# Kernel tuning notes

Hardware: AMD Instinct MI355X
Metric: run time of the kernel (lower is better)

The kernel has to match this reference:

```python
import jax, jax.numpy as jnp
import numpy as np

# ---- dims ----
V, VR, E, H, NF = 100000, 5000, 300, 256, 150
H2 = 2 * H  # 512


def _lstm_dir(x, Wih, Whh, b, h0, c0):
    # x: (T, B, E); returns hs (T, B, H), final (h, c)
    def step(carry, xt):
        h, c = carry
        z = xt @ Wih.T + h @ Whh.T + b
        i, f, g, o = jnp.split(z, 4, axis=-1)  # torch gate order i,f,g,o
        c = jax.nn.sigmoid(f) * c + jax.nn.sigmoid(i) * jnp.tanh(g)
        h = jax.nn.sigmoid(o) * jnp.tanh(c)
        return (h, c), h
    (hT, cT), hs = jax.lax.scan(step, (h0, c0), x)
    return hs, hT, cT


def bilstm(x, Wih_f, Whh_f, b_f, Wih_b, Whh_b, b_b, state=None):
    # x: (T, B, E) -> out (T, B, 2H), state tuple
    B = x.shape[1]
    if state is None:
        z = jnp.zeros((B, H), x.dtype)
        state = (z, z, z, z)
    h0f, c0f, h0b, c0b = state
    hs_f, hTf, cTf = _lstm_dir(x, Wih_f, Whh_f, b_f, h0f, c0f)
    hs_b, hTb, cTb = _lstm_dir(x[::-1], Wih_b, Whh_b, b_b, h0b, c0b)
    out = jnp.concatenate([hs_f, hs_b[::-1]], axis=-1)
    return out, (hTf, cTf, hTb, cTb)


def abwim_atten(question_out, word_rel, rela_rel, word_emb, rela_emb,
                Wih_f, Whh_f, b_f, Wih_b, Whh_b, b_b, W):
    # question_out: (B, 2H, Sq); word_rel (B,Sw), rela_rel (B,Sr) int
    rela = rela_emb[rela_rel.T]   # (Sr, B, E)
    word = word_emb[word_rel.T]   # (Sw, B, E)
    word_out, state = bilstm(word, Wih_f, Whh_f, b_f, Wih_b, Whh_b, b_b)
    rela_out, _ = bilstm(rela, Wih_f, Whh_f, b_f, Wih_b, Whh_b, b_b, state)
    relation = jnp.concatenate([rela_out, word_out], axis=0).transpose(1, 0, 2)  # (B, R, 2H)
    energy = jnp.einsum('brh,hk,bks->brs', relation, W, question_out)  # (B, R, Sq)
    B, R, Sq = energy.shape
    scale = 1.0 / np.sqrt(R).astype(np.float32)
    alpha = jax.nn.softmax(energy.reshape(B, R * Sq) * scale, axis=-1).reshape(B, R, Sq)
    # sum_r alpha[b,r,s] * relation[b,r,h] -> (B, 2H, Sq)
    return jnp.einsum('brs,brh->bhs', alpha, relation)


def setup_inputs():
    key = jax.random.key(0)
    ks = jax.random.split(key, 24)
    B, Sq, Sw, Sr = 64, 40, 12, 4
    s_emb, s_lstm, s_w = 0.05, 0.05, 0.04
    inp = {
        'question': jax.random.randint(ks[0], (B, Sq), 0, V),
        'word_relation': jax.random.randint(ks[1], (B, Sw), 0, V),
        'rela_relation': jax.random.randint(ks[2], (B, Sr), 0, VR),
        'word_previous': jax.random.randint(ks[3], (B, Sw), 0, V),
        'rela_previous': jax.random.randint(ks[4], (B, Sr), 0, VR),
        'word_emb': jax.random.normal(ks[5], (V, E), jnp.float32) * s_emb,
        'rela_emb': jax.random.normal(ks[6], (VR, E), jnp.float32) * s_emb,
        'Wih_f': jax.random.normal(ks[7], (4 * H, E), jnp.float32) * s_lstm,
        'Whh_f': jax.random.normal(ks[8], (4 * H, H), jnp.float32) * s_lstm,
        'b_f': jnp.zeros((4 * H,), jnp.float32),
        'Wih_b': jax.random.normal(ks[9], (4 * H, E), jnp.float32) * s_lstm,
        'Whh_b': jax.random.normal(ks[10], (4 * H, H), jnp.float32) * s_lstm,
        'b_b': jnp.zeros((4 * H,), jnp.float32),
        'W': jax.random.normal(ks[11], (H2, H2), jnp.float32) * s_w,
        'cnn1_w': jax.random.normal(ks[12], (NF, 2 * H2, 1), jnp.float32) * s_w,
        'cnn1_b': jnp.zeros((NF,), jnp.float32),
        'cnn2_w': jax.random.normal(ks[13], (NF, 2 * H2, 3), jnp.float32) * s_w,
        'cnn2_b': jnp.zeros((NF,), jnp.float32),
        'cnn3_w': jax.random.normal(ks[14], (NF, 2 * H2, 5), jnp.float32) * s_w,
        'cnn3_b': jnp.zeros((NF,), jnp.float32),
        'lin_w': jax.random.normal(ks[15], (1, NF), jnp.float32) * s_w,
        'lin2_w': jax.random.normal(ks[16], (H2, H2), jnp.float32) * s_w,
        'lin2_b': jnp.zeros((H2,), jnp.float32),
    }
    return inp


def _conv1d(x, w, b):
    # x: (B, C, L), w: (O, C, K)
    y = jax.lax.conv_general_dilated(x, w, (1,), 'VALID',
                                     dimension_numbers=('NCH', 'OIH', 'NCH'))
    return y + b[None, :, None]


def reference(question, word_relation, rela_relation, word_previous, rela_previous,
              word_emb, rela_emb, Wih_f, Whh_f, b_f, Wih_b, Whh_b, b_b, W,
              cnn1_w, cnn1_b, cnn2_w, cnn2_b, cnn3_w, cnn3_b, lin_w, lin2_w, lin2_b):
    lstm_p = (Wih_f, Whh_f, b_f, Wih_b, Whh_b, b_b)
    # question encoder (dropout is identity at eval)
    q = word_emb[question.T]                      # (Sq, B, E)
    q_out, _ = bilstm(q, *lstm_p)                 # (Sq, B, 2H)
    question_out = q_out.transpose(1, 2, 0)       # (B, 2H, Sq)
    # reduce one previous hop
    atten_prev = abwim_atten(question_out, word_previous, rela_previous,
                             word_emb, rela_emb, *lstm_p, W)
    qo = question_out - atten_prev
    qo = qo.transpose(0, 2, 1) @ lin2_w.T + lin2_b   # (B, Sq, 2H)
    question_out = qo.transpose(0, 2, 1)             # (B, 2H, Sq)
    # current relation attention
    atten_relation = abwim_atten(question_out, word_relation, rela_relation,
                                 word_emb, rela_emb, *lstm_p, W)
    M = jnp.concatenate([question_out, atten_relation], axis=1)  # (B, 4H, Sq)
    h1 = jnp.max(jax.nn.relu(_conv1d(M, cnn1_w, cnn1_b)), axis=2)  # (B, NF)
    h2 = jnp.max(jax.nn.relu(_conv1d(M, cnn2_w, cnn2_b)), axis=2)
    h3 = jnp.max(jax.nn.relu(_conv1d(M, cnn3_w, cnn3_b)), axis=2)
    h = jnp.maximum(jnp.maximum(h1, h2), h3)
    score = (h @ lin_w.T).squeeze(-1)  # (B,)
    return score
```

## Files before the change

### kernel.cpp

```cpp
#include <hip/hip_runtime.h>
#include <math.h>

#define NEG_INF (-3.402823466e+38f)

typedef __attribute__((ext_vector_type(8))) short short8;
typedef __attribute__((ext_vector_type(8))) unsigned short ushort8;
typedef __attribute__((ext_vector_type(4))) float f32x4;

constexpr int NTOK = 4608;
constexpr int BH = 64 * 256;

constexpr size_t OFF_WQ    = 0;
constexpr size_t OFF_B2    = OFF_WQ    + 524288;
constexpr size_t OFF_XB3T  = OFF_B2    + 2048;
constexpr size_t OFF_WB3T  = OFF_XB3T  + 983040;
constexpr size_t OFF_L2B3T = OFF_WB3T  + 393216;
constexpr size_t OFF_C1B3T = OFF_L2B3T + 393216;
constexpr size_t OFF_C2B3T = OFF_C1B3T + 294912;
constexpr size_t OFF_C3B3T = OFF_C2B3T + 884736;
constexpr size_t OFF_XHI   = OFF_C3B3T + 1474560;
constexpr size_t OFF_XLO   = OFF_XHI   + 737280;
constexpr size_t OFF_XP    = OFF_XLO   + 737280;
constexpr size_t OFF_HSQ   = OFF_XP    + 9437184;
constexpr size_t OFF_HSWP  = OFF_HSQ   + 1310720;
constexpr size_t OFF_HSRP  = OFF_HSWP  + 393216;
constexpr size_t OFF_HSWR  = OFF_HSRP  + 131072;
constexpr size_t OFF_HSRR  = OFF_HSWR  + 393216;
constexpr size_t OFF_CS    = OFF_HSRR  + 131072;
constexpr size_t OFF_RELP  = OFF_CS    + 163840;
constexpr size_t OFF_RELC  = OFF_RELP  + 524288;
constexpr size_t OFF_RELW  = OFF_RELC  + 524288;
constexpr size_t OFF_EN    = OFF_RELW  + 524288;

__device__ inline unsigned short f2bf(float f) {
  unsigned int u = __float_as_uint(f);
  u += 0x7FFFu + ((u >> 16) & 1u);
  return (unsigned short)(u >> 16);
}
__device__ inline float bf2f(unsigned short h) {
  return __uint_as_float(((unsigned int)h) << 16);
}
__device__ inline short8 mk8(unsigned long long a, unsigned long long b) {
  union { unsigned long long q[2]; short8 s; } u;
  u.q[0] = a; u.q[1] = b; return u.s;
}
#define ALD(p) __hip_atomic_load((p), __ATOMIC_RELAXED, __HIP_MEMORY_SCOPE_AGENT)
#define AST(p, v) __hip_atomic_store((p), (v), __ATOMIC_RELAXED, __HIP_MEMORY_SCOPE_AGENT)

__global__ __launch_bounds__(256) void k_prep(
    const float* __restrict__ Whh_f, const float* __restrict__ Whh_b,
    const float* __restrict__ b_f,   const float* __restrict__ b_b,
    const float* __restrict__ Wih_f, const float* __restrict__ Wih_b,
    const float* __restrict__ Wat,   const float* __restrict__ l2w,
    const float* __restrict__ c1w, const float* __restrict__ c2w, const float* __restrict__ c3w,
    unsigned short* __restrict__ WHB, float* __restrict__ B2,
    unsigned short* __restrict__ XB3T, unsigned short* __restrict__ WB3T,
    unsigned short* __restrict__ L2B3T,
    unsigned short* __restrict__ C1B3T, unsigned short* __restrict__ C2B3T,
    unsigned short* __restrict__ C3B3T, int* __restrict__ flags) {
  int idx = blockIdx.x * 256 + threadIdx.x;
  if (idx < 3072)
    AST(flags + idx * 16, 0);
  else if (idx < 3200)
    AST(flags + 49152 + (idx - 3072) * 16, 0);
  if (idx < 1048576) {
    int e = idx & 511;
    int k = e & 255, isLo = e >> 8;
    int row = (idx >> 9) & 63;
    int tile = (idx >> 15) & 15;
    int d = idx >> 19;
    int g = row >> 4, uu = row & 15;
    int u = tile * 16 + uu;
    const float* Wh = d ? Whh_b : Whh_f;
    float w = Wh[(size_t)(g * 256 + u) * 256 + k];
    unsigned short hi = f2bf(w);
    WHB[idx] = isLo ? f2bf(w - bf2f(hi)) : hi;
    return;
  }
  idx -= 1048576;
  if (idx < 2048) { B2[idx] = (idx < 1024) ? b_f[idx] : b_b[idx-1024]; return; }
  idx -= 2048;
  unsigned short* dst; int n, k, K;
  float w;
  if (idx < 655360) {
    n = idx / 320; k = idx % 320; K = 320; dst = XB3T;
    w = (k < 300) ? ((n < 1024) ? Wih_f[(size_t)n*300 + k] : Wih_b[(size_t)(n-1024)*300 + k]) : 0.f;
  } else if ((idx -= 655360) < 262144) {
    n = idx >> 9; k = idx & 511; K = 512; dst = WB3T;
    w = Wat[(size_t)k*512 + n];
  } else if ((idx -= 262144) < 262144) {
    n = idx >> 9; k = idx & 511; K = 512; dst = L2B3T;
    w = l2w[(size_t)n*512 + k];
  } else if ((idx -= 262144) < 196608) {
    n = idx >> 10; k = idx & 1023; K = 1024; dst = C1B3T;
    w = (n < 150) ? c1w[(size_t)n*1024 + k] : 0.f;
  } else if ((idx -= 196608) < 589824) {
    n = idx / 3072; k = idx % 3072; K = 3072; dst = C2B3T;
    int kw = k >> 10, c = k & 1023;
    w = (n < 150) ? c2w[((size_t)n*1024 + c)*3 + kw] : 0.f;
  } else if ((idx -= 589824) < 983040) {
    n = idx / 5120; k = idx % 5120; K = 5120; dst = C3B3T;
    int kw = k >> 10, c = k & 1023;
    w = (n < 150) ? c3w[((size_t)n*1024 + c)*5 + kw] : 0.f;
  } else return;
  unsigned short hi = f2bf(w);
  unsigned short lo = f2bf(w - bf2f(hi));
  size_t base = (size_t)n * (3*K);
  dst[base + k] = hi;
  dst[base + K + k] = lo;
  dst[base + 2*K + k] = hi;
}

__global__ __launch_bounds__(320) void k_gather(
    const int* __restrict__ q,  const int* __restrict__ wr, const int* __restrict__ rr,
    const int* __restrict__ wp, const int* __restrict__ rp,
    const float* __restrict__ we, const float* __restrict__ re,
    unsigned short* __restrict__ Xhi, unsigned short* __restrict__ Xlo) {
  int m = blockIdx.x, k = threadIdx.x;
  const float* emb; int row;
  if (m < 2560)      { int t=m>>6,    b=m&63; row = q [b*40+t]; emb = we; }
  else if (m < 3328) { int mm=m-2560; int t=mm>>6,b=mm&63; row = wp[b*12+t]; emb = we; }
  else if (m < 3584) { int mm=m-3328; int t=mm>>6,b=mm&63; row = rp[b*4 +t]; emb = re; }
  else if (m < 4352) { int mm=m-3584; int t=mm>>6,b=mm&63; row = wr[b*12+t]; emb = we; }
  else               { int mm=m-4352; int t=mm>>6,b=mm&63; row = rr[b*4 +t]; emb = re; }
  float v = (k < 300) ? emb[(size_t)row*300 + k] : 0.f;
  unsigned short hi = f2bf(v);
  Xhi[(size_t)m*320 + k] = hi;
  Xlo[(size_t)m*320 + k] = f2bf(v - bf2f(hi));
}

template<bool BIAS>
__global__ __launch_bounds__(256) void k_mgemm(
    const unsigned short* __restrict__ Ahi, const unsigned short* __restrict__ Alo, int lda,
    const unsigned short* __restrict__ Bt, const float* __restrict__ bias,
    float* __restrict__ C, int N, int K) {
  __shared__ unsigned short As[64 * 40];
  __shared__ unsigned short Bs[64 * 40];
  int tid = threadIdx.x;
  int wave = tid >> 6, lane = tid & 63;
  int quad = lane >> 4, l16 = lane & 15;
  int m0 = blockIdx.x << 6, n0 = blockIdx.y << 6;
  int K3 = 3 * K;
  int sr = tid >> 2;
  int sc = (tid & 3) << 3;
  f32x4 acc[4] = {};
  for (int k0 = 0; k0 < K3; k0 += 32) {
    int c = (k0 >= K) + (k0 >= 2*K);
    const unsigned short* Asrc = (c == 2) ? Alo : Ahi;
    int kk = k0 - c * K;
    ushort8 av = *(const ushort8*)(Asrc + (size_t)(m0 + sr) * lda + kk + sc);
    ushort8 bv = *(const ushort8*)(Bt + (size_t)(n0 + sr) * K3 + k0 + sc);
    *(ushort8*)&As[sr * 40 + sc] = av;
    *(ushort8*)&Bs[sr * 40 + sc] = bv;
    __syncthreads();
    short8 a  = *(const short8*)&As[(wave*16 + l16) * 40 + quad*8];
    short8 b0 = *(const short8*)&Bs[( 0 + l16) * 40 + quad*8];
    short8 b1 = *(const short8*)&Bs[(16 + l16) * 40 + quad*8];
    short8 b2 = *(const short8*)&Bs[(32 + l16) * 40 + quad*8];
    short8 b3 = *(const short8*)&Bs[(48 + l16) * 40 + quad*8];
    acc[0] = __builtin_amdgcn_mfma_f32_16x16x32_bf16(a, b0, acc[0], 0, 0, 0);
    acc[1] = __builtin_amdgcn_mfma_f32_16x16x32_bf16(a, b1, acc[1], 0, 0, 0);
    acc[2] = __builtin_amdgcn_mfma_f32_16x16x32_bf16(a, b2, acc[2], 0, 0, 0);
    acc[3] = __builtin_amdgcn_mfma_f32_16x16x32_bf16(a, b3, acc[3], 0, 0, 0);
    __syncthreads();
  }
  int row0 = m0 + wave * 16 + quad * 4;
#pragma unroll
  for (int t = 0; t < 4; t++) {
    int col = n0 + t * 16 + l16;
    float bb = BIAS ? bias[col] : 0.f;
#pragma unroll
    for (int r = 0; r < 4; r++)
      C[(size_t)(row0 + r) * N + col] = acc[t][r] + bb;
  }
}

__global__ __launch_bounds__(256) void k_cgemm(
    const unsigned short* __restrict__ Ahi, const unsigned short* __restrict__ Alo,
    const unsigned short* __restrict__ B1, const unsigned short* __restrict__ B2c,
    const unsigned short* __restrict__ B3,
    float* __restrict__ Y1, float* __restrict__ Y2, float* __restrict__ Y3) {
  __shared__ unsigned short As[64 * 40];
  __shared__ unsigned short Bs[64 * 40];
  int z = blockIdx.z;
  const unsigned short* Bt; float* Y; int K, sidx, chunk;
  if (z < 4)       { Bt = B1;  Y = Y1; K = 1024; sidx = z;      chunk = 768;  }
  else if (z < 12) { Bt = B2c; Y = Y2; K = 3072; sidx = z - 4;  chunk = 1152; }
  else             { Bt = B3;  Y = Y3; K = 5120; sidx = z - 12; chunk = 1920; }
  int K3 = 3 * K;
  int ks = sidx * chunk, ke = ks + chunk;
  int tid = threadIdx.x;
  int wave = tid >> 6, lane = tid & 63;
  int quad = lane >> 4, l16 = lane & 15;
  int m0 = blockIdx.x << 6, n0 = blockIdx.y << 6;
  int sr = tid >> 2;
  int sc = (tid & 3) << 3;
  f32x4 acc[4] = {};
  for (int k0 = ks; k0 < ke; k0 += 32) {
    int c = (k0 >= K) + (k0 >= 2*K);
    const unsigned short* Asrc = (c == 2) ? Alo : Ahi;
    int kk = k0 - c * K;
    ushort8 av = *(const ushort8*)(Asrc + (size_t)(m0 + sr) * 1024 + kk + sc);
    ushort8 bv = *(const ushort8*)(Bt + (size_t)(n0 + sr) * K3 + k0 + sc);
    *(ushort8*)&As[sr * 40 + sc] = av;
    *(ushort8*)&Bs[sr * 40 + sc] = bv;
    __syncthreads();
    short8 a  = *(const short8*)&As[(wave*16 + l16) * 40 + quad*8];
    short8 b0 = *(const short8*)&Bs[( 0 + l16) * 40 + quad*8];
    short8 b1 = *(const short8*)&Bs[(16 + l16) * 40 + quad*8];
    short8 b2 = *(const short8*)&Bs[(32 + l16) * 40 + quad*8];
    short8 b3 = *(const short8*)&Bs[(48 + l16) * 40 + quad*8];
    acc[0] = __builtin_amdgcn_mfma_f32_16x16x32_bf16(a, b0, acc[0], 0, 0, 0);
    acc[1] = __builtin_amdgcn_mfma_f32_16x16x32_bf16(a, b1, acc[1], 0, 0, 0);
    acc[2] = __builtin_amdgcn_mfma_f32_16x16x32_bf16(a, b2, acc[2], 0, 0, 0);
    acc[3] = __builtin_amdgcn_mfma_f32_16x16x32_bf16(a, b3, acc[3], 0, 0, 0);
    __syncthreads();
  }
  int row0 = m0 + wave * 16 + quad * 4;
#pragma unroll
  for (int t = 0; t < 4; t++) {
    int col = n0 + t * 16 + l16;
#pragma unroll
    for (int r = 0; r < 4; r++)
      atomicAdd(&Y[(size_t)(row0 + r) * 192 + col], acc[t][r]);
  }
}

__global__ __launch_bounds__(256) void k_zero(float* __restrict__ p, int n4) {
  int idx = blockIdx.x * 256 + threadIdx.x;
  if (idx < n4) *(float4*)(p + (size_t)idx * 4) = make_float4(0.f, 0.f, 0.f, 0.f);
}

__global__ __launch_bounds__(256, 1) void k_steps(
    const unsigned short* __restrict__ WHB, const float* __restrict__ XP,
    float* __restrict__ hsQ, float* __restrict__ hsWp, float* __restrict__ hsRp,
    float* __restrict__ hsWr, float* __restrict__ hsRr,
    unsigned short* HxA, unsigned short* HxB,
    int* flags, int* det) {
  int bid = blockIdx.x;
  int chain = bid & 7;
  if (chain >= 6) return;
  int tile = bid >> 3;
  int dir = chain & 1, fam = chain >> 1;
  int tid = threadIdx.x;
  int wave = tid >> 6, lane = tid & 63;
  int quad = lane >> 4, l16 = lane & 15;
  int u0 = tile << 4;

  unsigned myxcd;
  asm volatile("s_getreg_b32 %0, hwreg(HW_REG_XCC_ID)" : "=s"(myxcd));
  if (tid == 0) AST(det + bid * 16, (int)myxcd + 1);

  const unsigned short* wsrc = WHB + (((size_t)dir * 16 + tile) << 15);
  short8 Bh[4][8], Bl[4][8];
#pragma unroll
  for (int nf = 0; nf < 4; nf++)
#pragma unroll
    for (int j = 0; j < 8; j++) {
      const unsigned short* wr = wsrc + (nf * 16 + l16) * 512 + j * 32 + quad * 8;
      Bh[nf][j] = *(const short8*)(wr);
      Bl[nf][j] = *(const short8*)(wr + 256);
    }

  __shared__ int s_fast;
  int idv = 0;
  if (tid < 16) {
    const int* dp = det + (tid * 8 + chain) * 16;
    int v;
    while ((v = ALD(dp)) == 0) __builtin_amdgcn_s_sleep(1);
    idv = v;
  }
  if (wave == 0) {
    int ref = __shfl(idv, 0, 64);
    unsigned long long bad = __ballot((lane < 16) && (idv != ref));
    if (lane == 0) s_fast = (bad == 0ULL);
  }
  __syncthreads();
  int fast = s_fast;

  int nsteps = (fam == 0) ? 40 : 16;
  int slot0 = (chain < 2) ? chain * 40 : 80 + (chain - 2) * 16;
  float creg[4] = {0.f, 0.f, 0.f, 0.f};
  int roff = (quad * 64 + wave * 16 + l16) * 8;
  int wj = tile >> 1;
  int wq = ((tile & 1) << 1) + (l16 >> 3);
  int wbase = ((wj * 4 + wq) * 64) * 4 + ((l16 & 7) >> 1);

  for (int cs = 0; cs < nsteps; cs++) {
    int t, T, seg; float* hsb;
    if (fam == 0)     { t = cs;      T = 40; seg = 0;                         hsb = hsQ + (size_t)dir * 40 * BH; }
    else if (cs < 12) { t = cs;      T = 12; seg = (fam == 1) ? 2560 : 3584;  hsb = ((fam == 1) ? hsWp : hsWr) + (size_t)dir * 12 * BH; }
    else              { t = cs - 12; T = 4;  seg = (fam == 1) ? 3328 : 4352;  hsb = ((fam == 1) ? hsRp : hsRr) + (size_t)dir * 4 * BH; }
    int t_in = dir ? (T - 1 - t) : t;
    int u = u0 + l16;
    const float* xb = XP + (size_t)(seg + t_in * 64) * 2048 + dir * 1024 + u;
    float xi[4], xf[4], xg[4], xo[4];
#pragma unroll
    for (int r = 0; r < 4; r++) {
      const float* xr = xb + (size_t)(wave * 16 + quad * 4 + r) * 2048;
      xi[r] = xr[0]; xf[r] = xr[256]; xg[r] = xr[512]; xo[r] = xr[768];
    }

    f32x4 acc[4] = {};
    if (cs > 0) {
      int rs = slot0 + cs - 1;
      const unsigned short* Hb = (rs < 96) ? (HxA + (size_t)rs * 32768)
                                           : (HxB + (size_t)(rs - 96) * 32768);
      if (tid < 16) {
        const int* fp = flags + ((rs * 16 + tid) << 4);
        while (ALD(fp) == 0) __builtin_amdgcn_s_sleep(1);
      }
      __syncthreads();
      short8 ah[8], al[8];
      if (fast) {
#pragma unroll
        for (int j = 0; j < 8; j++) {
          ah[j] = *(const short8*)(Hb + j * 2048 + roff);
          al[j] = *(const short8*)(Hb + 16384 + j * 2048 + roff);
        }
      } else {
        const unsigned long long* ph = (const unsigned long long*)Hb;
        const unsigned long long* pl = ph + 4096;
        int r4 = roff >> 2;
        unsigned long long rv[32];
#pragma unroll
        for (int j = 0; j < 8; j++) { rv[2*j] = ALD(ph + j*512 + r4); rv[2*j+1] = ALD(ph + j*512 + r4 + 1); }
#pragma unroll
        for (int j = 0; j < 8; j++) { rv[16+2*j] = ALD(pl + j*512 + r4); rv[16+2*j+1] = ALD(pl + j*512 + r4 + 1); }
#pragma unroll
        for (int j = 0; j < 8; j++) { ah[j] = mk8(rv[2*j], rv[2*j+1]); al[j] = mk8(rv[16+2*j], rv[16+2*j+1]); }
      }
#pragma unroll
      for (int j = 0; j < 8; j++) {
        acc[0] = __builtin_amdgcn_mfma_f32_16x16x32_bf16(ah[j], Bh[0][j], acc[0], 0, 0, 0);
        acc[1] = __builtin_amdgcn_mfma_f32_16x16x32_bf16(ah[j], Bh[1][j], acc[1], 0, 0, 0);
        acc[2] = __builtin_amdgcn_mfma_f32_16x16x32_bf16(ah[j], Bh[2][j], acc[2], 0, 0, 0);
        acc[3] = __builtin_amdgcn_mfma_f32_16x16x32_bf16(ah[j], Bh[3][j], acc[3], 0, 0, 0);
      }
#pragma unroll
      for (int j = 0; j < 8; j++) {
        acc[0] = __builtin_amdgcn_mfma_f32_16x16x32_bf16(ah[j], Bl[0][j], acc[0], 0, 0, 0);
        acc[1] = __builtin_amdgcn_mfma_f32_16x16x32_bf16(ah[j], Bl[1][j], acc[1], 0, 0, 0);
        acc[2] = __builtin_amdgcn_mfma_f32_16x16x32_bf16(ah[j], Bl[2][j], acc[2], 0, 0, 0);
        acc[3] = __builtin_amdgcn_mfma_f32_16x16x32_bf16(ah[j], Bl[3][j], acc[3], 0, 0, 0);
      }
#pragma unroll
      for (int j = 0; j < 8; j++) {
        acc[0] = __builtin_amdgcn_mfma_f32_16x16x32_bf16(al[j], Bh[0][j], acc[0], 0, 0, 0);
        acc[1] = __builtin_amdgcn_mfma_f32_16x16x32_bf16(al[j], Bh[1][j], acc[1], 0, 0, 0);
        acc[2] = __builtin_amdgcn_mfma_f32_16x16x32_bf16(al[j], Bh[2][j], acc[2], 0, 0, 0);
        acc[3] = __builtin_amdgcn_mfma_f32_16x16x32_bf16(al[j], Bh[3][j], acc[3], 0, 0, 0);
      }
    }
    float hnv[4];
#pragma unroll
    for (int r = 0; r < 4; r++) {
      float zi = acc[0][r] + xi[r];
      float zf = acc[1][r] + xf[r];
      float zg = acc[2][r] + xg[r];
      float zo = acc[3][r] + xo[r];
      float gi = 1.f / (1.f + expf(-zi));
      float gf = 1.f / (1.f + expf(-zf));
      float go = 1.f / (1.f + expf(-zo));
      float gg = tanhf(zg);
      float cn = gf * creg[r] + gi * gg;
      hnv[r] = go * tanhf(cn);
      creg[r] = cn;
    }
    int wslot = slot0 + cs;
    if (cs + 1 < nsteps) {
      unsigned short* Ho = (wslot < 96) ? (HxA + (size_t)wslot * 32768)
                                        : (HxB + (size_t)(wslot - 96) * 32768);
      unsigned int* ohw = (unsigned int*)Ho + wbase;
      unsigned int* olw = (unsigned int*)(Ho + 16384) + wbase;
#pragma unroll
      for (int r = 0; r < 4; r++) {
        int b = wave * 16 + quad * 4 + r;
        unsigned short h16 = f2bf(hnv[r]);
        unsigned short l16v = f2bf(hnv[r] - bf2f(h16));
        unsigned int pk = (unsigned int)h16 | ((unsigned int)l16v << 16);
        unsigned int pw = (unsigned int)__shfl_xor((int)pk, 1, 64);
        if ((lane & 1) == 0) {
          unsigned int hw = (pk & 0xFFFFu) | (pw << 16);
          unsigned int lw = (pk >> 16) | (pw & 0xFFFF0000u);
          if (fast) { ohw[b * 4] = hw; olw[b * 4] = lw; }
          else      { AST(ohw + b * 4, hw); AST(olw + b * 4, lw); }
        }
      }
      __syncthreads();
      if (tid == 0)
        AST(flags + ((wslot * 16 + tile) << 4), 1);
    }
    float* hout = hsb + (size_t)t * BH + u;
#pragma unroll
    for (int r = 0; r < 4; r++) {
      int b = wave * 16 + quad * 4 + r;
      hout[(size_t)b * 256] = hnv[r];
    }
  }
}

__global__ __launch_bounds__(256) void k_qo1(const float* __restrict__ hsQ, float* __restrict__ QT) {
  int idx = blockIdx.x * 256 + threadIdx.x;
  if (idx >= 64*40*512) return;
  int h = idx & 511; int t2 = idx >> 9; int s = t2 % 40; int b = t2 / 40;
  float v;
  if (h < 256) v = hsQ[(size_t)s * BH + b*256 + h];
  else         v = hsQ[(size_t)40 * BH + (size_t)(39 - s) * BH + b*256 + (h - 256)];
  QT[idx] = v;
}

__global__ __launch_bounds__(256) void k_rel(
    const float* __restrict__ hsWp, const float* __restrict__ hsRp,
    const float* __restrict__ hsWr, const float* __restrict__ hsRr,
    float* __restrict__ RELP, float* __restrict__ RELC,
    unsigned short* __restrict__ RPhi, unsigned short* __restrict__ RPlo,
    unsigned short* __restrict__ RChi, unsigned short* __restrict__ RClo) {
  int idx0 = blockIdx.x * 256 + threadIdx.x;
  if (idx0 >= 2*64*16*512) return;
  int call = idx0 >= 64*16*512;
  int idx = idx0 - call * 64*16*512;
  int h = idx & 511; int t2 = idx >> 9; int r = t2 & 15; int b = t2 >> 4;
  const float* hsW = call ? hsWr : hsWp;
  const float* hsR = call ? hsRr : hsRp;
  float v;
  if (r < 4) {
    if (h < 256) v = hsR[(size_t)r * BH + b*256 + h];
    else         v = hsR[(size_t)4 * BH + (size_t)(3 - r) * BH + b*256 + (h - 256)];
  } else {
    int t = r - 4;
    if (h < 256) v = hsW[(size_t)t * BH + b*256 + h];
    else         v = hsW[(size_t)12 * BH + (size_t)(11 - t) * BH + b*256 + (h - 256)];
  }
  unsigned short hi = f2bf(v);
  unsigned short lo = f2bf(v - bf2f(hi));
  if (call) { RELC[idx] = v; RChi[idx] = hi; RClo[idx] = lo; }
  else      { RELP[idx] = v; RPhi[idx] = hi; RPlo[idx] = lo; }
}

__global__ __launch_bounds__(256) void k_energy(
    const float* __restrict__ relW, const float* __restrict__ QT, float* __restrict__ EN) {
  int idx = blockIdx.x * 256 + threadIdx.x;
  if (idx >= 64*16*40) return;
  int s = idx % 40; int t = idx / 40; int r = t & 15; int b = t >> 4;
  const float* rw = relW + (size_t)(b*16 + r) * 512;
  const float* qv = QT   + (size_t)(b*40 + s) * 512;
  float acc = 0.f;
#pragma unroll 4
  for (int k = 0; k < 512; k += 4) {
    float4 a = *(const float4*)(rw + k);
    float4 c = *(const float4*)(qv + k);
    acc += a.x*c.x + a.y*c.y + a.z*c.z + a.w*c.w;
  }
  EN[idx] = acc;
}

__global__ __launch_bounds__(256) void k_softmax(float* __restrict__ EN) {
  int b = blockIdx.x; int tid = threadIdx.x;
  float* e = EN + b * 640;
  float v0 = e[tid] * 0.25f, v1 = e[tid + 256] * 0.25f;
  float v2 = (tid < 128) ? e[tid + 512] * 0.25f : NEG_INF;
  __shared__ float sh[256];
  sh[tid] = fmaxf(v0, fmaxf(v1, v2));
  __syncthreads();
  for (int st = 128; st > 0; st >>= 1) { if (tid < st) sh[tid] = fmaxf(sh[tid], sh[tid+st]); __syncthreads(); }
  float m = sh[0];
  __syncthreads();
  float e0 = expf(v0 - m), e1 = expf(v1 - m);
  float e2 = (tid < 128) ? expf(v2 - m) : 0.f;
  sh[tid] = e0 + e1 + e2;
  __syncthreads();
  for (int st = 128; st > 0; st >>= 1) { if (tid < st) sh[tid] += sh[tid+st]; __syncthreads(); }
  float inv = 1.f / sh[0];
  e[tid] = e0 * inv; e[tid + 256] = e1 * inv;
  if (tid < 128) e[tid + 512] = e2 * inv;
}

__global__ __launch_bounds__(256) void k_atten(
    const float* __restrict__ AL, const float* __restrict__ REL, float* __restrict__ ATT) {
  int idx = blockIdx.x * 256 + threadIdx.x;
  if (idx >= 64*40*512) return;
  int h = idx & 511; int t2 = idx >> 9; int s = t2 % 40; int b = t2 / 40;
  const float* al = AL + b * 640 + s;
  const float* rl = REL + (size_t)b * 16 * 512 + h;
  float acc = 0.f;
#pragma unroll
  for (int r = 0; r < 16; r++) acc += al[r*40] * rl[r*512];
  ATT[idx] = acc;
}

__global__ __launch_bounds__(256) void k_sub(
    const float* __restrict__ QT, const float* __restrict__ ATT,
    unsigned short* __restrict__ Dhi, unsigned short* __restrict__ Dlo) {
  int idx = blockIdx.x * 256 + threadIdx.x;
  if (idx >= 64*40*512) return;
  float v = QT[idx] - ATT[idx];
  unsigned short hi = f2bf(v);
  Dhi[idx] = hi; Dlo[idx] = f2bf(v - bf2f(hi));
}

__global__ __launch_bounds__(256) void k_m2(
    const float* __restrict__ QO2, const float* __restrict__ ATT,
    unsigned short* __restrict__ M2hi, unsigned short* __restrict__ M2lo) {
  int idx = blockIdx.x * 256 + threadIdx.x;
  if (idx >= 2626048) return;
  float v = 0.f;
  if (idx < 2621440) {
    int c = idx & 1023; int m = idx >> 10;
    v = (c < 512) ? QO2[(size_t)m*512 + c] : ATT[(size_t)m*512 + (c - 512)];
  }
  unsigned short hi = f2bf(v);
  M2hi[idx] = hi; M2lo[idx] = f2bf(v - bf2f(hi));
}

__global__ __launch_bounds__(256) void k_pool(
    const float* __restrict__ Y1, const float* __restrict__ Y2, const float* __restrict__ Y3,
    const float* __restrict__ b1, const float* __restrict__ b2, const float* __restrict__ b3,
    const float* __restrict__ lw, float* __restrict__ out) {
  int b = blockIdx.x, o = threadIdx.x;
  float hv = 0.f;
  if (o < 150) {
    const float* y1 = Y1 + (size_t)b*40*192 + o;
    const float* y2 = Y2 + (size_t)b*40*192 + o;
    const float* y3 = Y3 + (size_t)b*40*192 + o;
    float m1 = NEG_INF, m2 = NEG_INF, m3 = NEG_INF;
#pragma unroll 4
    for (int l = 0; l < 40; l++) m1 = fmaxf(m1, y1[l*192]);
#pragma unroll 2
    for (int l = 0; l < 38; l++) m2 = fmaxf(m2, y2[l*192]);
#pragma unroll 2
    for (int l = 0; l < 36; l++) m3 = fmaxf(m3, y3[l*192]);
    float h = fmaxf(fmaxf(m1 + b1[o], m2 + b2[o]), m3 + b3[o]);
    hv = fmaxf(h, 0.f) * lw[o];
  }
  __shared__ float sh[256];
  sh[threadIdx.x] = hv;
  __syncthreads();
  for (int st = 128; st > 0; st >>= 1) { if (threadIdx.x < st) sh[threadIdx.x] += sh[threadIdx.x+st]; __syncthreads(); }
  if (threadIdx.x == 0) out[b] = sh[0];
}

extern "C" void kernel_launch(void* const* d_in, const int* in_sizes, int n_in,
                              void* d_out, int out_size, void* d_ws, size_t ws_size,
                              hipStream_t stream) {
  const int*   q    = (const int*)d_in[0];
  const int*   wrel = (const int*)d_in[1];
  const int*   rrel = (const int*)d_in[2];
  const int*   wprv = (const int*)d_in[3];
  const int*   rprv = (const int*)d_in[4];
  const float* we   = (const float*)d_in[5];
  const float* re   = (const float*)d_in[6];
  const float* Wih_f= (const float*)d_in[7];
  const float* Whh_f= (const float*)d_in[8];
  const float* b_f  = (const float*)d_in[9];
  const float* Wih_b= (const float*)d_in[10];
  const float* Whh_b= (const float*)d_in[11];
  const float* b_b  = (const float*)d_in[12];
  const float* W    = (const float*)d_in[13];
  const float* c1w  = (const float*)d_in[14];
  const float* c1b  = (const float*)d_in[15];
  const float* c2w  = (const float*)d_in[16];
  const float* c2b  = (const float*)d_in[17];
  const float* c3w  = (const float*)d_in[18];
  const float* c3b  = (const float*)d_in[19];
  const float* lw   = (const float*)d_in[20];
  const float* l2w  = (const float*)d_in[21];
  const float* l2b  = (const float*)d_in[22];
  float* out = (float*)d_out;
  float* ws  = (float*)d_ws;

  unsigned short* WHB = (unsigned short*)(ws + OFF_WQ);
  float* B2   = ws + OFF_B2;
  unsigned short* XB3T  = (unsigned short*)(ws + OFF_XB3T);
  unsigned short* WB3T  = (unsigned short*)(ws + OFF_WB3T);
  unsigned short* L2B3T = (unsigned short*)(ws + OFF_L2B3T);
  unsigned short* C1B3T = (unsigned short*)(ws + OFF_C1B3T);
  unsigned short* C2B3T = (unsigned short*)(ws + OFF_C2B3T);
  unsigned short* C3B3T = (unsigned short*)(ws + OFF_C3B3T);
  unsigned short* Xhi   = (unsigned short*)(ws + OFF_XHI);
  unsigned short* Xlo   = (unsigned short*)(ws + OFF_XLO);
  float* XP   = ws + OFF_XP;
  float* HSQ  = ws + OFF_HSQ;
  float* HSWP = ws + OFF_HSWP;
  float* HSRP = ws + OFF_HSRP;
  float* HSWR = ws + OFF_HSWR;
  float* HSRR = ws + OFF_HSRR;
  int*   flags = (int*)(ws + OFF_CS);
  int*   det   = flags + 49152;
  float* RELP = ws + OFF_RELP;
  float* RELC = ws + OFF_RELC;
  float* RELW = ws + OFF_RELW;
  float* EN   = ws + OFF_EN;
  unsigned short* HxA = (unsigned short*)(ws + OFF_RELP);
  unsigned short* HxB = (unsigned short*)(ws + OFF_XB3T);
  float* QO1  = XP;
  float* ATT  = XP + 1310720;
  float* QO2  = XP + 2621440;
  unsigned short* Dhi  = (unsigned short*)(XP + 3932160);
  unsigned short* Dlo  = (unsigned short*)(XP + 4587520);
  unsigned short* RPhi = (unsigned short*)(XP + 5242880);
  unsigned short* RPlo = (unsigned short*)(XP + 5505024);
  unsigned short* RChi = (unsigned short*)(XP + 5767168);
  unsigned short* RClo = (unsigned short*)(XP + 6029312);
  unsigned short* M2hi = (unsigned short*)(XP + 5242880);
  unsigned short* M2lo = (unsigned short*)(XP + 6555904);
  float* Y1   = XP + 7868928;
  float* Y2   = XP + 8360448;
  float* Y3   = XP + 8851968;

  k_prep<<<15624, 256, 0, stream>>>(Whh_f, Whh_b, b_f, b_b, Wih_f, Wih_b, W, l2w,
                                    c1w, c2w, c3w,
                                    WHB, B2, XB3T, WB3T, L2B3T, C1B3T, C2B3T, C3B3T, flags);
  k_gather<<<NTOK, 320, 0, stream>>>(q, wrel, rrel, wprv, rprv, we, re, Xhi, Xlo);
  { dim3 g(72, 32); k_mgemm<true><<<g, 256, 0, stream>>>(Xhi, Xlo, 320, XB3T, B2, XP, 2048, 320); }

  k_steps<<<128, 256, 0, stream>>>(WHB, XP, HSQ, HSWP, HSRP, HSWR, HSRR, HxA, HxB, flags, det);

  k_qo1<<<5120, 256, 0, stream>>>(HSQ, QO1);
  k_rel<<<4096, 256, 0, stream>>>(HSWP, HSRP, HSWR, HSRR, RELP, RELC, RPhi, RPlo, RChi, RClo);

  { dim3 g(16, 8); k_mgemm<false><<<g, 256, 0, stream>>>(RPhi, RPlo, 512, WB3T, nullptr, RELW, 512, 512); }
  k_energy<<<160, 256, 0, stream>>>(RELW, QO1, EN);
  k_softmax<<<64, 256, 0, stream>>>(EN);
  k_atten<<<5120, 256, 0, stream>>>(EN, RELP, ATT);
  k_sub<<<5120, 256, 0, stream>>>(QO1, ATT, Dhi, Dlo);
  { dim3 g(40, 8); k_mgemm<true><<<g, 256, 0, stream>>>(Dhi, Dlo, 512, L2B3T, l2b, QO2, 512, 512); }

  { dim3 g(16, 8); k_mgemm<false><<<g, 256, 0, stream>>>(RChi, RClo, 512, WB3T, nullptr, RELW, 512, 512); }
  k_energy<<<160, 256, 0, stream>>>(RELW, QO2, EN);
  k_softmax<<<64, 256, 0, stream>>>(EN);
  k_atten<<<5120, 256, 0, stream>>>(EN, RELC, ATT);

  k_m2<<<10258, 256, 0, stream>>>(QO2, ATT, M2hi, M2lo);
  k_zero<<<1440, 256, 0, stream>>>(Y1, 368640);
  { dim3 g(40, 3, 20); k_cgemm<<<g, 256, 0, stream>>>(M2hi, M2lo, C1B3T, C2B3T, C3B3T, Y1, Y2, Y3); }
  k_pool<<<64, 256, 0, stream>>>(Y1, Y2, Y3, c1b, c2b, c3b, lw, out);
}
```

Measured before the change: 687.8 us.

## Restructure conv as per-tap GEMM and use 128x128 tiled bgemm

```diff
diff --git a/kernel.cpp b/kernel.cpp
--- a/kernel.cpp
+++ b/kernel.cpp
@@ -15,10 +15,8 @@
 constexpr size_t OFF_XB3T  = OFF_B2    + 2048;
 constexpr size_t OFF_WB3T  = OFF_XB3T  + 983040;
 constexpr size_t OFF_L2B3T = OFF_WB3T  + 393216;
-constexpr size_t OFF_C1B3T = OFF_L2B3T + 393216;
-constexpr size_t OFF_C2B3T = OFF_C1B3T + 294912;
-constexpr size_t OFF_C3B3T = OFF_C2B3T + 884736;
-constexpr size_t OFF_XHI   = OFF_C3B3T + 1474560;
+constexpr size_t OFF_CB3T  = OFF_L2B3T + 393216;
+constexpr size_t OFF_XHI   = OFF_CB3T  + 2654208;
 constexpr size_t OFF_XLO   = OFF_XHI   + 737280;
 constexpr size_t OFF_XP    = OFF_XLO   + 737280;
 constexpr size_t OFF_HSQ   = OFF_XP    + 9437184;
@@ -55,9 +53,8 @@
     const float* __restrict__ c1w, const float* __restrict__ c2w, const float* __restrict__ c3w,
     unsigned short* __restrict__ WHB, float* __restrict__ B2,
     unsigned short* __restrict__ XB3T, unsigned short* __restrict__ WB3T,
-    unsigned short* __restrict__ L2B3T,
-    unsigned short* __restrict__ C1B3T, unsigned short* __restrict__ C2B3T,
-    unsigned short* __restrict__ C3B3T, int* __restrict__ flags) {
+    unsigned short* __restrict__ L2B3T, unsigned short* __restrict__ CB3T,
+    int* __restrict__ flags) {
   int idx = blockIdx.x * 256 + threadIdx.x;
   if (idx < 3072)
     AST(flags + idx * 16, 0);
@@ -91,17 +88,14 @@
   } else if ((idx -= 262144) < 262144) {
     n = idx >> 9; k = idx & 511; K = 512; dst = L2B3T;
     w = l2w[(size_t)n*512 + k];
-  } else if ((idx -= 262144) < 196608) {
-    n = idx >> 10; k = idx & 1023; K = 1024; dst = C1B3T;
-    w = (n < 150) ? c1w[(size_t)n*1024 + k] : 0.f;
-  } else if ((idx -= 196608) < 589824) {
-    n = idx / 3072; k = idx % 3072; K = 3072; dst = C2B3T;
-    int kw = k >> 10, c = k & 1023;
-    w = (n < 150) ? c2w[((size_t)n*1024 + c)*3 + kw] : 0.f;
-  } else if ((idx -= 589824) < 983040) {
-    n = idx / 5120; k = idx % 5120; K = 5120; dst = C3B3T;
-    int kw = k >> 10, c = k & 1023;
-    w = (n < 150) ? c3w[((size_t)n*1024 + c)*5 + kw] : 0.f;
+  } else if ((idx -= 262144) < 1441792) {
+    n = idx >> 10; k = idx & 1023; K = 1024; dst = CB3T;
+    if (n < 1350) {
+      int t = n / 150, o = n % 150;
+      w = (t == 0) ? c1w[(size_t)o*1024 + k]
+        : (t < 4)  ? c2w[((size_t)o*1024 + k)*3 + (t-1)]
+                   : c3w[((size_t)o*1024 + k)*5 + (t-4)];
+    } else w = 0.f;
   } else return;
   unsigned short hi = f2bf(w);
   unsigned short lo = f2bf(w - bf2f(hi));
@@ -175,60 +169,62 @@
   }
 }
 
-__global__ __launch_bounds__(256) void k_cgemm(
-    const unsigned short* __restrict__ Ahi, const unsigned short* __restrict__ Alo,
-    const unsigned short* __restrict__ B1, const unsigned short* __restrict__ B2c,
-    const unsigned short* __restrict__ B3,
-    float* __restrict__ Y1, float* __restrict__ Y2, float* __restrict__ Y3) {
-  __shared__ unsigned short As[64 * 40];
-  __shared__ unsigned short Bs[64 * 40];
-  int z = blockIdx.z;
-  const unsigned short* Bt; float* Y; int K, sidx, chunk;
-  if (z < 4)       { Bt = B1;  Y = Y1; K = 1024; sidx = z;      chunk = 768;  }
-  else if (z < 12) { Bt = B2c; Y = Y2; K = 3072; sidx = z - 4;  chunk = 1152; }
-  else             { Bt = B3;  Y = Y3; K = 5120; sidx = z - 12; chunk = 1920; }
-  int K3 = 3 * K;
-  int ks = sidx * chunk, ke = ks + chunk;
+template<bool BIAS>
+__global__ __launch_bounds__(256) void k_bgemm(
+    const unsigned short* __restrict__ Ahi, const unsigned short* __restrict__ Alo, int lda,
+    const unsigned short* __restrict__ Bt, const float* __restrict__ bias,
+    float* __restrict__ C, int N, int K) {
+  __shared__ unsigned short As[128 * 64];
+  __shared__ unsigned short Bs[128 * 64];
   int tid = threadIdx.x;
   int wave = tid >> 6, lane = tid & 63;
   int quad = lane >> 4, l16 = lane & 15;
-  int m0 = blockIdx.x << 6, n0 = blockIdx.y << 6;
-  int sr = tid >> 2;
-  int sc = (tid & 3) << 3;
-  f32x4 acc[4] = {};
-  for (int k0 = ks; k0 < ke; k0 += 32) {
+  int wm = wave >> 1, wn = wave & 1;
+  int m0 = blockIdx.x << 7, n0 = blockIdx.y << 7;
+  int K3 = 3 * K;
+  f32x4 acc[4][4] = {};
+  for (int k0 = 0; k0 < K3; k0 += 64) {
     int c = (k0 >= K) + (k0 >= 2*K);
     const unsigned short* Asrc = (c == 2) ? Alo : Ahi;
     int kk = k0 - c * K;
-    ushort8 av = *(const ushort8*)(Asrc + (size_t)(m0 + sr) * 1024 + kk + sc);
-    ushort8 bv = *(const ushort8*)(Bt + (size_t)(n0 + sr) * K3 + k0 + sc);
-    *(ushort8*)&As[sr * 40 + sc] = av;
-    *(ushort8*)&Bs[sr * 40 + sc] = bv;
+#pragma unroll
+    for (int j = 0; j < 4; j++) {
+      int ci = j * 256 + tid;
+      int r = ci >> 3, c8 = (ci & 7) << 3;
+      ushort8 av = *(const ushort8*)(Asrc + (size_t)(m0 + r) * lda + kk + c8);
+      ushort8 bv = *(const ushort8*)(Bt + (size_t)(n0 + r) * K3 + k0 + c8);
+      *(ushort8*)&As[ci * 8] = av;
+      *(ushort8*)&Bs[ci * 8] = bv;
+    }
     __syncthreads();
-    short8 a  = *(const short8*)&As[(wave*16 + l16) * 40 + quad*8];
-    short8 b0 = *(const short8*)&Bs[( 0 + l16) * 40 + quad*8];
-    short8 b1 = *(const short8*)&Bs[(16 + l16) * 40 + quad*8];
-    short8 b2 = *(const short8*)&Bs[(32 + l16) * 40 + quad*8];
-    short8 b3 = *(const short8*)&Bs[(48 + l16) * 40 + quad*8];
-    acc[0] = __builtin_amdgcn_mfma_f32_16x16x32_bf16(a, b0, acc[0], 0, 0, 0);
-    acc[1] = __builtin_amdgcn_mfma_f32_16x16x32_bf16(a, b1, acc[1], 0, 0, 0);
-    acc[2] = __builtin_amdgcn_mfma_f32_16x16x32_bf16(a, b2, acc[2], 0, 0, 0);
-    acc[3] = __builtin_amdgcn_mfma_f32_16x16x32_bf16(a, b3, acc[3], 0, 0, 0);
+#pragma unroll
+    for (int s = 0; s < 2; s++) {
+      short8 af[4], bf[4];
+#pragma unroll
+      for (int f = 0; f < 4; f++) {
+        af[f] = *(const short8*)&As[(wm*64 + f*16 + l16) * 64 + s*32 + quad*8];
+        bf[f] = *(const short8*)&Bs[(wn*64 + f*16 + l16) * 64 + s*32 + quad*8];
+      }
+#pragma unroll
+      for (int fm = 0; fm < 4; fm++)
+#pragma unroll
+        for (int fn = 0; fn < 4; fn++)
+          acc[fm][fn] = __builtin_amdgcn_mfma_f32_16x16x32_bf16(af[fm], bf[fn], acc[fm][fn], 0, 0, 0);
+    }
     __syncthreads();
   }
-  int row0 = m0 + wave * 16 + quad * 4;
-#pragma unroll
-  for (int t = 0; t < 4; t++) {
-    int col = n0 + t * 16 + l16;
-#pragma unroll
-    for (int r = 0; r < 4; r++)
-      atomicAdd(&Y[(size_t)(row0 + r) * 192 + col], acc[t][r]);
-  }
-}
-
-__global__ __launch_bounds__(256) void k_zero(float* __restrict__ p, int n4) {
-  int idx = blockIdx.x * 256 + threadIdx.x;
-  if (idx < n4) *(float4*)(p + (size_t)idx * 4) = make_float4(0.f, 0.f, 0.f, 0.f);
+#pragma unroll
+  for (int fm = 0; fm < 4; fm++) {
+    int row0 = m0 + wm*64 + fm*16 + quad*4;
+#pragma unroll
+    for (int fn = 0; fn < 4; fn++) {
+      int col = n0 + wn*64 + fn*16 + l16;
+      float bb = BIAS ? bias[col] : 0.f;
+#pragma unroll
+      for (int r = 0; r < 4; r++)
+        C[(size_t)(row0 + r) * N + col] = acc[fm][fn][r] + bb;
+    }
+  }
 }
 
 __global__ __launch_bounds__(256, 1) void k_steps(
@@ -514,22 +510,25 @@
 }
 
 __global__ __launch_bounds__(256) void k_pool(
-    const float* __restrict__ Y1, const float* __restrict__ Y2, const float* __restrict__ Y3,
+    const float* __restrict__ Y,
     const float* __restrict__ b1, const float* __restrict__ b2, const float* __restrict__ b3,
     const float* __restrict__ lw, float* __restrict__ out) {
   int b = blockIdx.x, o = threadIdx.x;
   float hv = 0.f;
   if (o < 150) {
-    const float* y1 = Y1 + (size_t)b*40*192 + o;
-    const float* y2 = Y2 + (size_t)b*40*192 + o;
-    const float* y3 = Y3 + (size_t)b*40*192 + o;
+    const float* yb = Y + (size_t)b * 40 * 1408 + o;
     float m1 = NEG_INF, m2 = NEG_INF, m3 = NEG_INF;
 #pragma unroll 4
-    for (int l = 0; l < 40; l++) m1 = fmaxf(m1, y1[l*192]);
+    for (int l = 0; l < 40; l++) m1 = fmaxf(m1, yb[l*1408]);
 #pragma unroll 2
-    for (int l = 0; l < 38; l++) m2 = fmaxf(m2, y2[l*192]);
+    for (int l = 0; l < 38; l++)
+      m2 = fmaxf(m2, yb[l*1408 + 150] + yb[(l+1)*1408 + 300] + yb[(l+2)*1408 + 450]);
 #pragma unroll 2
-    for (int l = 0; l < 36; l++) m3 = fmaxf(m3, y3[l*192]);
+    for (int l = 0; l < 36; l++) {
+      float s = yb[l*1408 + 600] + yb[(l+1)*1408 + 750] + yb[(l+2)*1408 + 900]
+              + yb[(l+3)*1408 + 1050] + yb[(l+4)*1408 + 1200];
+      m3 = fmaxf(m3, s);
+    }
     float h = fmaxf(fmaxf(m1 + b1[o], m2 + b2[o]), m3 + b3[o]);
     hv = fmaxf(h, 0.f) * lw[o];
   }
@@ -574,9 +573,7 @@
   unsigned short* XB3T  = (unsigned short*)(ws + OFF_XB3T);
   unsigned short* WB3T  = (unsigned short*)(ws + OFF_WB3T);
   unsigned short* L2B3T = (unsigned short*)(ws + OFF_L2B3T);
-  unsigned short* C1B3T = (unsigned short*)(ws + OFF_C1B3T);
-  unsigned short* C2B3T = (unsigned short*)(ws + OFF_C2B3T);
-  unsigned short* C3B3T = (unsigned short*)(ws + OFF_C3B3T);
+  unsigned short* CB3T  = (unsigned short*)(ws + OFF_CB3T);
   unsigned short* Xhi   = (unsigned short*)(ws + OFF_XHI);
   unsigned short* Xlo   = (unsigned short*)(ws + OFF_XLO);
   float* XP   = ws + OFF_XP;
@@ -604,15 +601,13 @@
   unsigned short* RClo = (unsigned short*)(XP + 6029312);
   unsigned short* M2hi = (unsigned short*)(XP + 5242880);
   unsigned short* M2lo = (unsigned short*)(XP + 6555904);
-  float* Y1   = XP + 7868928;
-  float* Y2   = XP + 8360448;
-  float* Y3   = XP + 8851968;
-
-  k_prep<<<15624, 256, 0, stream>>>(Whh_f, Whh_b, b_f, b_b, Wih_f, Wih_b, W, l2w,
+  float* Y    = XP;
+
+  k_prep<<<14344, 256, 0, stream>>>(Whh_f, Whh_b, b_f, b_b, Wih_f, Wih_b, W, l2w,
                                     c1w, c2w, c3w,
-                                    WHB, B2, XB3T, WB3T, L2B3T, C1B3T, C2B3T, C3B3T, flags);
+                                    WHB, B2, XB3T, WB3T, L2B3T, CB3T, flags);
   k_gather<<<NTOK, 320, 0, stream>>>(q, wrel, rrel, wprv, rprv, we, re, Xhi, Xlo);
-  { dim3 g(72, 32); k_mgemm<true><<<g, 256, 0, stream>>>(Xhi, Xlo, 320, XB3T, B2, XP, 2048, 320); }
+  { dim3 g(36, 16); k_bgemm<true><<<g, 256, 0, stream>>>(Xhi, Xlo, 320, XB3T, B2, XP, 2048, 320); }
 
   k_steps<<<128, 256, 0, stream>>>(WHB, XP, HSQ, HSWP, HSRP, HSWR, HSRR, HxA, HxB, flags, det);
 
@@ -632,7 +627,6 @@
   k_atten<<<5120, 256, 0, stream>>>(EN, RELC, ATT);
 
   k_m2<<<10258, 256, 0, stream>>>(QO2, ATT, M2hi, M2lo);
-  k_zero<<<1440, 256, 0, stream>>>(Y1, 368640);
-  { dim3 g(40, 3, 20); k_cgemm<<<g, 256, 0, stream>>>(M2hi, M2lo, C1B3T, C2B3T, C3B3T, Y1, Y2, Y3); }
-  k_pool<<<64, 256, 0, stream>>>(Y1, Y2, Y3, c1b, c2b, c3b, lw, out);
-}
+  { dim3 g(20, 11); k_bgemm<false><<<g, 256, 0, stream>>>(M2hi, M2lo, 1024, CB3T, nullptr, Y, 1408, 1024); }
+  k_pool<<<64, 256, 0, stream>>>(Y, c1b, c2b, c3b, lw, out);
+}
```

New measurement: 669.2 us. -2.7%, faster.
